# Performance work log

Measured on AMD Instinct MI355X. Metric: run time of the kernel, lower is better.

## Reference

```python
import jax, jax.numpy as jnp
import numpy as np

# Config: B=16, channels C=16, feature_num D=4, node_num K=128, L=128, emb E=10
# c_in for the 1x1 conv = (order*support_len + 1) * C = (2*3 + 1)*16 = 112

def setup_inputs() -> dict:
    key = jax.random.key(0)
    ks = jax.random.split(key, 8)
    B, C, D, K, L, E = 16, 16, 4, 128, 128, 10
    return {
        "x": jax.random.normal(ks[0], (B, C, D * K * L), dtype=jnp.float32),
        "supports": jax.random.uniform(ks[1], (2, K, K), dtype=jnp.float32),
        "nodevec1": jax.random.normal(ks[2], (D, K, E), dtype=jnp.float32),
        "nodevec2": jax.random.normal(ks[3], (D, E, K), dtype=jnp.float32),
        "imp_W": jax.random.normal(ks[4], (K, K), dtype=jnp.float32) * 0.05,
        "imp_b": jax.random.normal(ks[5], (K,), dtype=jnp.float32) * 0.05,
        "mlp_W": jax.random.normal(ks[6], (D, C, 7 * C), dtype=jnp.float32) * 0.05,
        "mlp_b": jax.random.normal(ks[7], (D, C), dtype=jnp.float32) * 0.05,
        "B": B, "C": C, "D": D, "K": K, "L": L,
    }


def reference(x, supports, nodevec1, nodevec2, imp_W, imp_b, mlp_W, mlp_b, B, C, D, K, L):
    # x: (B, C, D*K*L) -> (D, B*L, C, K)  [matches reshape/permute in torch forward]
    xr = x.reshape(B, C, D, K, L).transpose(2, 0, 4, 1, 3).reshape(D, B * L, C, K)

    # adaptive adjacency per feature
    # torch: importance = Linear(nv1.T).T  => imp[j,e] = sum_k W[j,k] nv1[k,e] + b[j]
    imp = jnp.einsum('jk,fke->fje', imp_W, nodevec1) + imp_b[None, :, None]
    nv1m = nodevec1 * imp                                   # (D, K, E)
    scores = jnp.einsum('fke,fej->fkj', nv1m, nodevec2)     # (D, K, K)
    adp = jax.nn.softmax(jax.nn.relu(scores), axis=2)       # softmax over dim=1 of (K,K)

    # multi-hop diffusion: out[n,c,w] = sum_v x[n,c,v] * a[w,v], order=2
    outs = [xr]
    for s in range(2):  # two shared supports
        a = supports[s]
        x1 = jnp.einsum('fncv,wv->fncw', xr, a)
        x2 = jnp.einsum('fncv,wv->fncw', x1, a)
        outs.append(x1)
        outs.append(x2)
    x1 = jnp.einsum('fncv,fwv->fncw', xr, adp)  # per-feature adaptive support
    x2 = jnp.einsum('fncv,fwv->fncw', x1, adp)
    outs.append(x1)
    outs.append(x2)

    cat = jnp.concatenate(outs, axis=2)  # (D, B*L, 7C, K)

    # per-feature 1x1 conv = channel GEMM
    y = jnp.einsum('fnck,foc->fnok', cat, mlp_W) + mlp_b[:, None, :, None]  # (D, N, C, K)

    y = y.reshape(D, B, L, C, K)
    y = jnp.transpose(y, (1, 2, 0, 3, 4))  # (B, L, D, C, K) == torch.stack(res, dim=2)
    y = jnp.transpose(y, (0, 3, 2, 4, 1))  # (B, C, D, K, L)
    return y.reshape(B, C, D * K * L)
```

## Files before the change

### kernel.cpp

```cpp
#include <hip/hip_runtime.h>


namespace {

constexpr int Kn = 128;
constexpr int En = 10;

typedef __attribute__((ext_vector_type(8))) short short8;
typedef __attribute__((ext_vector_type(4))) float f32x4;

__device__ inline unsigned short f2bf(float f) {
    unsigned x = __float_as_uint(f);
    return (unsigned short)((x + 0x7FFFu + ((x >> 16) & 1u)) >> 16);
}
__device__ inline unsigned pack2(float lo, float hi) {
    return (unsigned)f2bf(lo) | ((unsigned)f2bf(hi) << 16);
}

__global__ __launch_bounds__(256) void build_adj(
    const float* __restrict__ supports,
    const float* __restrict__ nv1,
    const float* __restrict__ nv2,
    const float* __restrict__ impW,
    const float* __restrict__ impB,
    float* __restrict__ mats)
{
    const int tid = threadIdx.x;
    const int blk = blockIdx.x;
    if (blk < 2) {
        const float* A = supports + blk * Kn * Kn;
        float* dst = mats + (blk * 2) * Kn * Kn;
        for (int i = tid; i < Kn * Kn; i += 256) dst[i] = A[i];
        return;
    }
    const int d = blk - 2;
    __shared__ float nv1m[Kn * En];
    __shared__ float nv2s[En * Kn];
    for (int i = tid; i < Kn * En; i += 256) nv1m[i] = nv1[d * Kn * En + i];
    for (int i = tid; i < En * Kn; i += 256) nv2s[i] = nv2[d * En * Kn + i];
    __syncthreads();
    float impv[5];
    #pragma unroll
    for (int r = 0; r < 5; ++r) {
        const int idx = tid + r * 256;
        const int j = idx / En, e = idx - j * En;
        float acc = impB[j];
        for (int kk = 0; kk < Kn; ++kk)
            acc += impW[j * Kn + kk] * nv1m[kk * En + e];
        impv[r] = acc;
    }
    __syncthreads();
    #pragma unroll
    for (int r = 0; r < 5; ++r) nv1m[tid + r * 256] *= impv[r];
    __syncthreads();
    if (tid < Kn) {
        const int k = tid;
        float a[En];
        #pragma unroll
        for (int e = 0; e < En; ++e) a[e] = nv1m[k * En + e];
        float mx = 0.f;
        for (int j = 0; j < Kn; ++j) {
            float s = 0.f;
            #pragma unroll
            for (int e = 0; e < En; ++e) s += a[e] * nv2s[e * Kn + j];
            mx = fmaxf(mx, s);
        }
        float sum = 0.f;
        for (int j = 0; j < Kn; ++j) {
            float s = 0.f;
            #pragma unroll
            for (int e = 0; e < En; ++e) s += a[e] * nv2s[e * Kn + j];
            s = fmaxf(s, 0.f);
            sum += expf(s - mx);
        }
        const float inv = 1.f / sum;
        float* dst = mats + (4 + d) * Kn * Kn;
        for (int j = 0; j < Kn; ++j) {
            float s = 0.f;
            #pragma unroll
            for (int e = 0; e < En; ++e) s += a[e] * nv2s[e * Kn + j];
            s = fmaxf(s, 0.f);
            dst[k * Kn + j] = expf(s - mx) * inv;
        }
    }
}

__global__ __launch_bounds__(256) void square_cvt(
    const float* __restrict__ fm, unsigned short* __restrict__ wbm)
{
    const int tid = threadIdx.x;
    if (blockIdx.x < 96) {
        __shared__ float S[Kn * Kn];
        const int m = blockIdx.x >> 4, strip = blockIdx.x & 15;
        const int src = (m == 0) ? 0 : (m == 1) ? 2 : (2 + m);
        const int dst = (m == 0) ? 2 : (m == 1) ? 4 : (2 + 2 * m);
        const float* s = fm + src * Kn * Kn;
        unsigned short* o = wbm + dst * Kn * Kn;
        for (int i = tid; i < Kn * Kn; i += 256) S[i] = s[i];
        __syncthreads();
        const int v = strip * 8 + (tid >> 5);
        const int k0 = (tid & 31) * 4;
        float acc0 = 0.f, acc1 = 0.f, acc2 = 0.f, acc3 = 0.f;
        for (int u0 = 0; u0 < Kn; u0 += 4) {
            const float4 av = *reinterpret_cast<const float4*>(&S[v * Kn + u0]);
            const float a[4] = {av.x, av.y, av.z, av.w};
            #pragma unroll
            for (int j = 0; j < 4; ++j) {
                const float4 m4 = *reinterpret_cast<const float4*>(&S[(u0 + j) * Kn + k0]);
                acc0 += a[j] * m4.x; acc1 += a[j] * m4.y;
                acc2 += a[j] * m4.z; acc3 += a[j] * m4.w;
            }
        }
        uint2 r;
        r.x = pack2(acc0, acc1);
        r.y = pack2(acc2, acc3);
        *reinterpret_cast<uint2*>(&o[v * Kn + k0]) = r;
    } else {
        const int s = blockIdx.x - 96;
        const int wslot = (s == 0) ? 0 : (s == 1) ? 1 : (s == 2) ? 3 : (5 + 2 * (s - 3));
        const int fsrc  = (s == 0) ? -1 : (s == 1) ? 0 : (s == 2) ? 2 : (4 + (s - 3));
        for (int i = tid; i < Kn * Kn; i += 256) {
            const int k = i >> 7, v = i & 127;
            const float val = (fsrc < 0) ? ((k == v) ? 1.f : 0.f) : fm[fsrc * 16384 + i];
            wbm[wslot * 16384 + i] = f2bf(val);
        }
    }
}

__global__ __launch_bounds__(256, 2) void fused_mfma(
    const float* __restrict__ x,
    const unsigned short* __restrict__ wbm,
    const float* __restrict__ mlpW,
    const float* __restrict__ mlpB,
    float* __restrict__ out)
{
    __shared__ __align__(16) char lds[32768];
    const int tid = threadIdx.x;
    const int lane = tid & 63, lr = lane & 15, lg = lane >> 4;
    const int wid = tid >> 6, wr = wid >> 1, wk = wid & 1;

    const unsigned u = blockIdx.x;
    const unsigned pid = (u & 7) * 256 + (u >> 3);
    const int kh = pid & 1;
    const int lt = (pid >> 1) & 15;
    const int b  = (pid >> 5) & 15;
    const int d  = (int)(pid >> 9);
    const int l0 = lt * 8;

    const f32x4 zero4 = {0.f, 0.f, 0.f, 0.f};
    short8 Mb[8];
    const unsigned short* mbase = wbm + kh * 8192 + wk * 4096 + lr * 128 + lg * 8;

    auto loadM = [&](int slot) {
        const unsigned short* mp = mbase + slot * 16384;
        #pragma unroll
        for (int j = 0; j < 2; ++j)
            #pragma unroll
            for (int ks = 0; ks < 4; ++ks)
                Mb[j * 4 + ks] =
                    *reinterpret_cast<const short8*>(mp + j * 2048 + ks * 32);
    };

    loadM(0);

    {
        const int half = tid & 1;
        const int p5 = (tid >> 1) & 31;
        #pragma unroll
        for (int i = 0; i < 8; ++i) {
            const int g = i * 4 + wid;
            const int c = g >> 1, pg = g & 1;
            const int p = pg * 32 + p5;
            const int v = p * 2;
            const float* p0 = x + (size_t)b * 1048576 + c * 65536 + d * 16384 +
                              v * 128 + l0 + half * 4;
            const float4 q0 = *reinterpret_cast<const float4*>(p0);
            const float4 q1 = *reinterpret_cast<const float4*>(p0 + 128);
            const float a0[4] = {q0.x, q0.y, q0.z, q0.w};
            const float a1[4] = {q1.x, q1.y, q1.z, q1.w};
            const int colb = (4 * p) ^ ((c & 7) << 4);
            #pragma unroll
            for (int j = 0; j < 4; ++j) {
                const int n = half * 4 + j;
                *reinterpret_cast<unsigned*>(lds + (n * 16 + c) * 256 + colb) =
                    pack2(a0[j], a1[j]);
            }
        }
    }

    short8 Wf[4];
    #pragma unroll
    for (int p = 0; p < 4; ++p) {
        short8 w;
        #pragma unroll
        for (int j = 0; j < 8; ++j) {
            const int tc = lg * 8 + j, t = 2 * p + (tc >> 4), c = tc & 15;
            const float wv = (t < 7) ? mlpW[d * 1792 + lr * 112 + t * 16 + c] : 0.f;
            w[j] = (short)f2bf(wv);
        }
        Wf[p] = w;
    }

    __syncthreads();

    short8 Xf[4][4];
    {
        const int swz = (lr & 7) << 4;
        #pragma unroll
        for (int rti = 0; rti < 4; ++rti) {
            const int base = ((wr * 4 + rti) * 16 + lr) * 256;
            #pragma unroll
            for (int ks = 0; ks < 4; ++ks)
                Xf[rti][ks] = *reinterpret_cast<const short8*>(
                    lds + base + ((ks * 64 + lg * 16) ^ swz));
        }
    }
    __syncthreads();

    f32x4 Y[4][2];
    #pragma unroll
    for (int ni = 0; ni < 4; ++ni)
        #pragma unroll
        for (int kt = 0; kt < 2; ++kt) Y[ni][kt] = zero4;

    auto phaseA_Z = [&](int tp, bool zeroTail) {
        f32x4 D[4][2];
        #pragma unroll
        for (int rti = 0; rti < 4; ++rti) { D[rti][0] = zero4; D[rti][1] = zero4; }
        #pragma unroll
        for (int ks = 0; ks < 4; ++ks) {
            #pragma unroll
            for (int rti = 0; rti < 4; ++rti) {
                D[rti][0] = __builtin_amdgcn_mfma_f32_16x16x32_bf16(
                    Xf[rti][ks], Mb[ks], D[rti][0], 0, 0, 0);
                D[rti][1] = __builtin_amdgcn_mfma_f32_16x16x32_bf16(
                    Xf[rti][ks], Mb[4 + ks], D[rti][1], 0, 0, 0);
            }
        }
        #pragma unroll
        for (int rti = 0; rti < 4; ++rti) {
            #pragma unroll
            for (int j = 0; j < 2; ++j) {
                const int n = wr * 4 + rti;
                const int kp = (wk * 2 + j) * 16 + lr;
                uint2 zz;
                zz.x = pack2(D[rti][j][0], D[rti][j][1]);
                zz.y = pack2(D[rti][j][2], D[rti][j][3]);
                *reinterpret_cast<uint2*>(
                    lds + n * 4096 + ((kp * 64 + tp * 32 + lg * 8) ^ ((kp & 7) << 4))) = zz;
                if (zeroTail) {
                    const uint2 z0 = {0u, 0u};
                    *reinterpret_cast<uint2*>(
                        lds + n * 4096 + ((kp * 64 + 32 + lg * 8) ^ ((kp & 7) << 4))) = z0;
                }
            }
        }
    };

    auto phaseB = [&](const short8& Wfp) {
        #pragma unroll
        for (int ni = 0; ni < 4; ++ni) {
            const int n = wr * 4 + ni;
            #pragma unroll
            for (int ktl = 0; ktl < 2; ++ktl) {
                const int kp = wk * 32 + ktl * 16 + lr;
                const short8 Bfz = *reinterpret_cast<const short8*>(
                    lds + n * 4096 + ((kp * 64 + lg * 16) ^ ((kp & 7) << 4)));
                Y[ni][ktl] = __builtin_amdgcn_mfma_f32_16x16x32_bf16(
                    Wfp, Bfz, Y[ni][ktl], 0, 0, 0);
            }
        }
    };

    phaseA_Z(0, false);  loadM(1);
    phaseA_Z(1, false);  loadM(2);
    phaseB(Wf[0]);
    phaseA_Z(0, false);  loadM(3);
    phaseA_Z(1, false);  loadM(4);
    phaseB(Wf[1]);
    phaseA_Z(0, false);  loadM(5 + 2 * d);
    phaseA_Z(1, false);  loadM(6 + 2 * d);
    phaseB(Wf[2]);
    phaseA_Z(0, true);
    phaseB(Wf[3]);

    __syncthreads();

    #pragma unroll
    for (int ni = 0; ni < 4; ++ni) {
        const int l = wr * 4 + ni;
        #pragma unroll
        for (int ktl = 0; ktl < 2; ++ktl) {
            const int k = wk * 32 + ktl * 16 + lr;
            #pragma unroll
            for (int r = 0; r < 4; ++r) {
                const int o = lg * 4 + r;
                *reinterpret_cast<float*>(
                    lds + o * 2048 + k * 32 + ((l * 4) ^ (k & 12))) = Y[ni][ktl][r];
            }
        }
    }
    __syncthreads();

    {
        const int half = tid & 1;
        const int klo = (tid >> 1) & 31;
        #pragma unroll
        for (int i = 0; i < 8; ++i) {
            const int g = i * 4 + wid;
            const int o = g >> 1, kg = g & 1;
            const int k = kg * 32 + klo;
            const int pp = (k >> 2) & 3;
            const float4 F = *reinterpret_cast<const float4*>(
                lds + o * 2048 + k * 32 + half * 16);
            float4 s1, s2;
            if (pp & 1) { s1.x = F.y; s1.y = F.x; s1.z = F.w; s1.w = F.z; }
            else        { s1 = F; }
            if (pp & 2) { s2.x = s1.z; s2.y = s1.w; s2.z = s1.x; s2.w = s1.y; }
            else        { s2 = s1; }
            const float bv = mlpB[d * 16 + o];
            s2.x += bv; s2.y += bv; s2.z += bv; s2.w += bv;
            float* gp = out + (size_t)b * 1048576 + o * 65536 + d * 16384 +
                        (kh * 64 + k) * 128 + l0 + half * 4;
            *reinterpret_cast<float4*>(gp) = s2;
        }
    }
}

}

extern "C" void kernel_launch(void* const* d_in, const int* in_sizes, int n_in,
                              void* d_out, int out_size, void* d_ws, size_t ws_size,
                              hipStream_t stream)
{
    const float* x    = (const float*)d_in[0];
    const float* sup  = (const float*)d_in[1];
    const float* nv1  = (const float*)d_in[2];
    const float* nv2  = (const float*)d_in[3];
    const float* impW = (const float*)d_in[4];
    const float* impB = (const float*)d_in[5];
    const float* mlpW = (const float*)d_in[6];
    const float* mlpB = (const float*)d_in[7];
    float* outp = (float*)d_out;

    float* fm = (float*)d_ws;
    unsigned short* wbm = (unsigned short*)((char*)d_ws + 786432);

    build_adj<<<6, 256, 0, stream>>>(sup, nv1, nv2, impW, impB, fm);
    square_cvt<<<103, 256, 0, stream>>>(fm, wbm);
    fused_mfma<<<2048, 256, 0, stream>>>(x, wbm, mlpW, mlpB, outp);
}
```

Measured before the change: 141.5 us.

## Stream X fragments from LDS and raise occupancy to three blocks per CU

Drops the register-resident X fragments so they are re-read from LDS on every phase-A pass, and raises the launch bound to three blocks per CU. Phase B now runs after every phase-A pass into a separate Z buffer: the weight fragment is masked by half, and lanes whose weights are masked read from a small zeroed LDS area. The float-to-bf16 packing now uses the HIP intrinsic instead of hand-written rounding. The aim is lower register pressure for higher occupancy, paid for with more LDS reads, twice as many phase-B MFMAs, and a larger LDS footprint (about 48 KB per block). With three blocks that is about 144 KB, which may not fit per CU and could stop the occupancy target from being met.

```diff
diff --git a/kernel.cpp b/kernel.cpp
--- a/kernel.cpp
+++ b/kernel.cpp
@@ -1,4 +1,5 @@
 #include <hip/hip_runtime.h>
+#include <hip/hip_bf16.h>
 
 
 namespace {
@@ -15,6 +16,12 @@
 }
 __device__ inline unsigned pack2(float lo, float hi) {
     return (unsigned)f2bf(lo) | ((unsigned)f2bf(hi) << 16);
+}
+__device__ inline unsigned pack2b(float lo, float hi) {
+    union { __hip_bfloat162 h; unsigned u; } cv;
+    float2 f; f.x = lo; f.y = hi;
+    cv.h = __float22bfloat162_rn(f);
+    return cv.u;
 }
 
 __global__ __launch_bounds__(256) void build_adj(
@@ -127,14 +134,14 @@
     }
 }
 
-__global__ __launch_bounds__(256, 2) void fused_mfma(
+__global__ __launch_bounds__(256, 3) void fused_mfma(
     const float* __restrict__ x,
     const unsigned short* __restrict__ wbm,
     const float* __restrict__ mlpW,
     const float* __restrict__ mlpB,
     float* __restrict__ out)
 {
-    __shared__ __align__(16) char lds[32768];
+    __shared__ __align__(16) char lds[49216];
     const int tid = threadIdx.x;
     const int lane = tid & 63, lr = lane & 15, lg = lane >> 4;
     const int wid = tid >> 6, wr = wid >> 1, wk = wid & 1;
@@ -183,10 +190,11 @@
             for (int j = 0; j < 4; ++j) {
                 const int n = half * 4 + j;
                 *reinterpret_cast<unsigned*>(lds + (n * 16 + c) * 256 + colb) =
-                    pack2(a0[j], a1[j]);
-            }
-        }
-    }
+                    pack2b(a0[j], a1[j]);
+            }
+        }
+    }
+    if (tid < 8) *reinterpret_cast<unsigned*>(lds + 49152 + tid * 4) = 0u;
 
     short8 Wf[4];
     #pragma unroll
@@ -203,38 +211,30 @@
 
     __syncthreads();
 
-    short8 Xf[4][4];
-    {
-        const int swz = (lr & 7) << 4;
-        #pragma unroll
-        for (int rti = 0; rti < 4; ++rti) {
-            const int base = ((wr * 4 + rti) * 16 + lr) * 256;
-            #pragma unroll
-            for (int ks = 0; ks < 4; ++ks)
-                Xf[rti][ks] = *reinterpret_cast<const short8*>(
-                    lds + base + ((ks * 64 + lg * 16) ^ swz));
-        }
-    }
-    __syncthreads();
+    const int xrow = wr * 16384 + lr * 256;
+    const int xcol = (lg * 16) ^ ((lr & 7) << 4);
+    char* zb = lds + 32768;
 
     f32x4 Y[4][2];
     #pragma unroll
-    for (int ni = 0; ni < 4; ++ni)
-        #pragma unroll
-        for (int kt = 0; kt < 2; ++kt) Y[ni][kt] = zero4;
-
-    auto phaseA_Z = [&](int tp, bool zeroTail) {
+    for (int ni = 0; ni < 4; ++ni) {
+        Y[ni][0] = zero4; Y[ni][1] = zero4;
+    }
+
+    auto phaseA_Z = [&]() {
         f32x4 D[4][2];
         #pragma unroll
         for (int rti = 0; rti < 4; ++rti) { D[rti][0] = zero4; D[rti][1] = zero4; }
         #pragma unroll
         for (int ks = 0; ks < 4; ++ks) {
+            const char* xaddr = lds + xrow + (xcol ^ (ks * 64));
             #pragma unroll
             for (int rti = 0; rti < 4; ++rti) {
+                const short8 Xk = *reinterpret_cast<const short8*>(xaddr + rti * 4096);
                 D[rti][0] = __builtin_amdgcn_mfma_f32_16x16x32_bf16(
-                    Xf[rti][ks], Mb[ks], D[rti][0], 0, 0, 0);
+                    Xk, Mb[ks], D[rti][0], 0, 0, 0);
                 D[rti][1] = __builtin_amdgcn_mfma_f32_16x16x32_bf16(
-                    Xf[rti][ks], Mb[4 + ks], D[rti][1], 0, 0, 0);
+                    Xk, Mb[4 + ks], D[rti][1], 0, 0, 0);
             }
         }
         #pragma unroll
@@ -244,45 +244,43 @@
                 const int n = wr * 4 + rti;
                 const int kp = (wk * 2 + j) * 16 + lr;
                 uint2 zz;
-                zz.x = pack2(D[rti][j][0], D[rti][j][1]);
-                zz.y = pack2(D[rti][j][2], D[rti][j][3]);
-                *reinterpret_cast<uint2*>(
-                    lds + n * 4096 + ((kp * 64 + tp * 32 + lg * 8) ^ ((kp & 7) << 4))) = zz;
-                if (zeroTail) {
-                    const uint2 z0 = {0u, 0u};
-                    *reinterpret_cast<uint2*>(
-                        lds + n * 4096 + ((kp * 64 + 32 + lg * 8) ^ ((kp & 7) << 4))) = z0;
-                }
+                zz.x = pack2b(D[rti][j][0], D[rti][j][1]);
+                zz.y = pack2b(D[rti][j][2], D[rti][j][3]);
+                *reinterpret_cast<uint2*>(zb + n * 2048 + kp * 32 + lg * 8) = zz;
             }
         }
     };
 
-    auto phaseB = [&](const short8& Wfp) {
+    auto phaseB = [&](int p, int parity) {
+        short8 Wm;
+        const bool keep_lo = (parity == 0);
+        #pragma unroll
+        for (int j = 0; j < 8; ++j)
+            Wm[j] = ((lg < 2) == keep_lo) ? Wf[p][j] : (short)0;
+        const bool data_lane = ((lg < 2) == keep_lo);
         #pragma unroll
         for (int ni = 0; ni < 4; ++ni) {
             const int n = wr * 4 + ni;
             #pragma unroll
             for (int ktl = 0; ktl < 2; ++ktl) {
                 const int kp = wk * 32 + ktl * 16 + lr;
-                const short8 Bfz = *reinterpret_cast<const short8*>(
-                    lds + n * 4096 + ((kp * 64 + lg * 16) ^ ((kp & 7) << 4)));
+                const char* zp = data_lane
+                    ? (zb + n * 2048 + kp * 32 + (lg & 1) * 16)
+                    : (lds + 49152 + (lg & 1) * 16);
+                const short8 Bfz = *reinterpret_cast<const short8*>(zp);
                 Y[ni][ktl] = __builtin_amdgcn_mfma_f32_16x16x32_bf16(
-                    Wfp, Bfz, Y[ni][ktl], 0, 0, 0);
+                    Wm, Bfz, Y[ni][ktl], 0, 0, 0);
             }
         }
     };
 
-    phaseA_Z(0, false);  loadM(1);
-    phaseA_Z(1, false);  loadM(2);
-    phaseB(Wf[0]);
-    phaseA_Z(0, false);  loadM(3);
-    phaseA_Z(1, false);  loadM(4);
-    phaseB(Wf[1]);
-    phaseA_Z(0, false);  loadM(5 + 2 * d);
-    phaseA_Z(1, false);  loadM(6 + 2 * d);
-    phaseB(Wf[2]);
-    phaseA_Z(0, true);
-    phaseB(Wf[3]);
+    phaseA_Z();  loadM(1);          phaseB(0, 0);
+    phaseA_Z();  loadM(2);          phaseB(0, 1);
+    phaseA_Z();  loadM(3);          phaseB(1, 0);
+    phaseA_Z();  loadM(4);          phaseB(1, 1);
+    phaseA_Z();  loadM(5 + 2 * d);  phaseB(2, 0);
+    phaseA_Z();  loadM(6 + 2 * d);  phaseB(2, 1);
+    phaseA_Z();                     phaseB(3, 0);
 
     __syncthreads();
 
```

New measurement: 139.3 us. About the same (-1.5%).
